# Kernel tuning notes

Hardware: AMD Instinct MI355X
Metric: run time of the kernel (lower is better)

## Reference

```python
import jax, jax.numpy as jnp
import numpy as np

B, L, D = 256, 256, 128          # batch, max_len, embedding_dim
H = W = 16                       # H=int(sqrt(L)), W=L//H
N, CBD = 128, 1024               # embedding_num, code_book_dim = N*8 = D*8
BETA = 0.25
BN_EPS = 1e-3                    # tf.layers.batch_normalization default


def _conv(x, w, b):
    return jax.lax.conv_general_dilated(x, w, (1, 1), 'VALID',
        dimension_numbers=('NHWC', 'HWIO', 'NHWC')) + b


def _convT(x, w, b):
    return jax.lax.conv_transpose(x, w, (1, 1), 'VALID',
        dimension_numbers=('NHWC', 'HWIO', 'NHWC')) + b


def _bn(x, g, b):
    # inference-mode BN with moving_mean=0, moving_var=1 (tf.layers default training=False)
    return g * (x * (1.0 / np.sqrt(1.0 + BN_EPS))) + b


def setup_inputs() -> dict:
    key = jax.random.key(0)
    ks = jax.random.split(key, 24)
    rn = lambda k, s, sc=0.05: (jax.random.normal(k, s, dtype=jnp.float32) * sc)
    inp = {
        'x': jax.random.normal(ks[0], (B, L, D), dtype=jnp.float32),
        'mask': jnp.ones((B, L), dtype=jnp.float32),
        'code_book': jax.random.normal(ks[1], (N, CBD), dtype=jnp.float32),
        # encoder: conv2d k=2 valid, channels D -> 2D -> 4D -> 8D
        'ew1': rn(ks[2], (2, 2, D, 2 * D)), 'eb1': jnp.zeros((2 * D,), jnp.float32),
        'eg1': jnp.ones((2 * D,), jnp.float32), 'ebt1': jnp.zeros((2 * D,), jnp.float32),
        'ew2': rn(ks[3], (2, 2, 2 * D, 4 * D)), 'eb2': jnp.zeros((4 * D,), jnp.float32),
        'eg2': jnp.ones((4 * D,), jnp.float32), 'ebt2': jnp.zeros((4 * D,), jnp.float32),
        'ew3': rn(ks[4], (2, 2, 4 * D, 8 * D)), 'eb3': jnp.zeros((8 * D,), jnp.float32),
        # decoder: conv2d_transpose k=2 valid, channels 8D -> 4D -> 2D -> D
        'dw1': rn(ks[5], (2, 2, 8 * D, 4 * D)), 'db1': jnp.zeros((4 * D,), jnp.float32),
        'dg1': jnp.ones((4 * D,), jnp.float32), 'dbt1': jnp.zeros((4 * D,), jnp.float32),
        'dw2': rn(ks[6], (2, 2, 4 * D, 2 * D)), 'db2': jnp.zeros((2 * D,), jnp.float32),
        'dg2': jnp.ones((2 * D,), jnp.float32), 'dbt2': jnp.zeros((2 * D,), jnp.float32),
        'dw3': rn(ks[7], (2, 2, 2 * D, D)), 'db3': jnp.zeros((D,), jnp.float32),
    }
    return inp


def reference(x, mask, code_book,
              ew1, eb1, eg1, ebt1, ew2, eb2, eg2, ebt2, ew3, eb3,
              dw1, db1, dg1, dbt1, dw2, db2, dg2, dbt2, dw3, db3):
    # ---- encoder (conv branch) ----
    xi = x.reshape(-1, H, W, D)                                   # [B,16,16,D]
    h = jax.nn.relu(_bn(_conv(xi, ew1, eb1), eg1, ebt1))          # [B,15,15,2D]
    h = jax.nn.relu(_bn(_conv(h, ew2, eb2), eg2, ebt2))           # [B,14,14,4D]
    x_encode = _conv(h, ew3, eb3)                                 # [B,13,13,8D]

    # ---- VQ codebook lookup (get_quantized) ----
    flat = x_encode.reshape(-1, CBD)                              # [B*169, CBD]
    dist = (jnp.sum(flat ** 2, axis=1, keepdims=True)
            + jnp.sum(code_book ** 2, axis=1)
            - 2.0 * flat @ code_book.T)                           # [B*169, N]
    idx = jnp.argmin(dist, axis=1)
    quantized = code_book[idx].reshape(x_encode.shape)            # gather == one_hot @ code_book

    # ---- straight-through + decoder ----
    ste = x_encode + jax.lax.stop_gradient(quantized - x_encode)
    h = jax.nn.relu(_bn(_convT(ste, dw1, db1), dg1, dbt1))        # [B,14,14,4D]
    h = jax.nn.relu(_bn(_convT(h, dw2, db2), dg2, dbt2))          # [B,15,15,2D]
    vq = _convT(h, dw3, db3)                                      # [B,16,16,D]
    vq_x = vq.reshape(-1, L, D)

    vq_mean = jnp.sum(vq_x, axis=1) / jnp.sum(mask, axis=-1, keepdims=True)

    recon = jnp.mean((x - vq_x) ** 2)
    vq_l = jnp.mean((quantized - jax.lax.stop_gradient(x_encode)) ** 2)
    commit = jnp.mean((x_encode - jax.lax.stop_gradient(quantized)) ** 2)
    vqvae_loss = recon + vq_l + BETA * commit
    return (vq_mean, vq_x, x_encode, quantized, vqvae_loss)
```

## Files before the change

### kernel.cpp

```cpp
#include <hip/hip_runtime.h>
#include <math.h>

typedef float f4 __attribute__((ext_vector_type(4)));
typedef short s8 __attribute__((ext_vector_type(8)));

#define WS_FLOATS 66000000L
__device__ float g_fallback[WS_FLOATS];

__device__ __forceinline__ f4 ldg4(const float* p) { return *(const f4*)p; }

__device__ __forceinline__ unsigned short bfr(float x) {
    unsigned int u = __float_as_uint(x);
    u += 0x7fffu + ((u >> 16) & 1u);
    return (unsigned short)(u >> 16);
}
__device__ __forceinline__ float bff(unsigned short h) {
    return __uint_as_float(((unsigned int)h) << 16);
}
__device__ __forceinline__ s8 z8() { s8 z = {0,0,0,0,0,0,0,0}; return z; }

__device__ __forceinline__ void split8(const f4& x0, const f4& x1, s8& hi, s8& lo) {
#pragma unroll
    for (int e = 0; e < 4; ++e) {
        unsigned short h0 = bfr(x0[e]);
        hi[e] = (short)h0; lo[e] = (short)bfr(x0[e] - bff(h0));
        unsigned short h1 = bfr(x1[e]);
        hi[e + 4] = (short)h1; lo[e + 4] = (short)bfr(x1[e] - bff(h1));
    }
}

__global__ __launch_bounds__(512, 2)
void e2_gemm(const short* __restrict__ aHi, const short* __restrict__ aLo,
             const short* __restrict__ wHi, const short* __restrict__ wLo,
             const float* __restrict__ bias, const float* __restrict__ gamma,
             const float* __restrict__ beta,
             short* __restrict__ oHi, short* __restrict__ oLo, float bns)
{
    extern __shared__ short smem[];
    const int tid = threadIdx.x;
    const int w = tid >> 6, l = tid & 63;
    const int fr = l & 15, fq = l >> 4;
    const int wm = (w >> 2) * 128;
    const int wn = (w & 3) * 32;

    int m0, n0;
    {
        const int nwg = gridDim.x;
        const int bid = blockIdx.x;
        const int q = nwg >> 3, r = nwg & 7;
        const int xcd = bid & 7, c = bid >> 3;
        const int wg = (xcd < r ? xcd * (q + 1) : r * (q + 1) + (xcd - r) * q) + c;
        m0 = (wg >> 2) * 256;
        n0 = (wg & 3) * 128;
    }

    int aBase[2], aSwz[2], aDst[2];
#pragma unroll
    for (int i = 0; i < 2; ++i) {
        int p = tid + 512 * i;
        int row = p >> 2, ch = p & 3;
        int m = m0 + row;
        int b = m / 196; int rem = m - b * 196;
        int oi = rem / 14, oj = rem - oi * 14;
        aBase[i] = ((b * 15 + oi) * 15 + oj) * 256;
        aSwz[i] = (ch ^ (row & 3)) << 3;
        aDst[i] = row * 32 + ch * 8;
    }
    const int bRow = tid >> 2, bch = tid & 3;
    const int bSrcO = (n0 + bRow) * 1024 + ((bch ^ (bRow & 3)) << 3);
    const int bDst = bRow * 32 + bch * 8;

    auto stage = [&](int sel, int kc) {
        const int t = kc >> 8;
        const int toff = ((t >> 1) * 15 + (t & 1)) * 256 + (kc & 255);
#pragma unroll
        for (int i = 0; i < 2; ++i) {
            __builtin_amdgcn_global_load_lds(
                (const __attribute__((address_space(1))) void*)(aHi + aBase[i] + toff + aSwz[i]),
                (__attribute__((address_space(3))) void*)(smem + sel * 8192 + aDst[i]), 16, 0, 0);
            __builtin_amdgcn_global_load_lds(
                (const __attribute__((address_space(1))) void*)(aLo + aBase[i] + toff + aSwz[i]),
                (__attribute__((address_space(3))) void*)(smem + 16384 + sel * 8192 + aDst[i]), 16, 0, 0);
        }
        __builtin_amdgcn_global_load_lds(
            (const __attribute__((address_space(1))) void*)(wHi + bSrcO + kc),
            (__attribute__((address_space(3))) void*)(smem + 32768 + sel * 4096 + bDst), 16, 0, 0);
        __builtin_amdgcn_global_load_lds(
            (const __attribute__((address_space(1))) void*)(wLo + bSrcO + kc),
            (__attribute__((address_space(3))) void*)(smem + 40960 + sel * 4096 + bDst), 16, 0, 0);
    };

    f4 acc[8][2];
#pragma unroll
    for (int a = 0; a < 8; ++a)
#pragma unroll
        for (int b = 0; b < 2; ++b) acc[a][b] = (f4){0.f, 0.f, 0.f, 0.f};

    stage(0, 0);
    stage(1, 32);

    for (int t = 0; t < 32; ++t) {
        const int sel = t & 1;
        if (t < 31) asm volatile("s_waitcnt vmcnt(6)" ::: "memory");
        else        asm volatile("s_waitcnt vmcnt(0)" ::: "memory");
        __builtin_amdgcn_s_barrier();
        __builtin_amdgcn_sched_barrier(0);

        const short* Ah = smem + sel * 8192;
        const short* Al = smem + 16384 + sel * 8192;
        const short* Bh = smem + 32768 + sel * 4096;
        const short* Bl = smem + 40960 + sel * 4096;

        s8 afh[8], afl[8], bfh[2], bfl[2];
#pragma unroll
        for (int mf = 0; mf < 8; ++mf) {
            int ar = wm + mf * 16 + fr;
            int ao = ar * 32 + ((fq ^ (ar & 3)) << 3);
            afh[mf] = *(const s8*)&Ah[ao];
            afl[mf] = *(const s8*)&Al[ao];
        }
#pragma unroll
        for (int nf = 0; nf < 2; ++nf) {
            int br = wn + nf * 16 + fr;
            int bo = br * 32 + ((fq ^ (br & 3)) << 3);
            bfh[nf] = *(const s8*)&Bh[bo];
            bfl[nf] = *(const s8*)&Bl[bo];
        }
        asm volatile("s_waitcnt lgkmcnt(0)" ::: "memory");
        __builtin_amdgcn_sched_barrier(0);
        __builtin_amdgcn_s_barrier();
        __builtin_amdgcn_sched_barrier(0);
        if (t + 2 < 32) stage(sel, (t + 2) * 32);

        __builtin_amdgcn_s_setprio(1);
#pragma unroll
        for (int mf = 0; mf < 8; ++mf)
#pragma unroll
            for (int nf = 0; nf < 2; ++nf) {
                acc[mf][nf] = __builtin_amdgcn_mfma_f32_16x16x32_bf16(
                    afh[mf], bfh[nf], acc[mf][nf], 0, 0, 0);
                acc[mf][nf] = __builtin_amdgcn_mfma_f32_16x16x32_bf16(
                    afh[mf], bfl[nf], acc[mf][nf], 0, 0, 0);
                acc[mf][nf] = __builtin_amdgcn_mfma_f32_16x16x32_bf16(
                    afl[mf], bfh[nf], acc[mf][nf], 0, 0, 0);
            }
        __builtin_amdgcn_s_setprio(0);
    }

    float bi2[2], ga[2], be[2];
#pragma unroll
    for (int nf = 0; nf < 2; ++nf) {
        int col = n0 + wn + nf * 16 + fr;
        bi2[nf] = bias[col]; ga[nf] = gamma[col]; be[nf] = beta[col];
    }
#pragma unroll
    for (int mf = 0; mf < 8; ++mf)
#pragma unroll
        for (int j = 0; j < 4; ++j) {
            long gm = m0 + wm + mf * 16 + fq * 4 + j;
#pragma unroll
            for (int nf = 0; nf < 2; ++nf) {
                float v = ga[nf] * ((acc[mf][nf][j] + bi2[nf]) * bns) + be[nf];
                v = fmaxf(v, 0.f);
                long o = gm * 512 + n0 + wn + nf * 16 + fr;
                unsigned short h = bfr(v);
                oHi[o] = (short)h;
                oLo[o] = (short)bfr(v - bff(h));
            }
        }
}

template<int EPI>
__global__ __launch_bounds__(512, 2)
void gemm256(const short* __restrict__ aSrc, const short* __restrict__ wHi,
             const float* __restrict__ bias, const float* __restrict__ gamma,
             const float* __restrict__ beta, void* __restrict__ oHi,
             double* __restrict__ sacc, const short* __restrict__ zsrc,
             int IH, int IW, int OHOW, int OW, int N, int K, int off,
             int ntShift, float bns)
{
    extern __shared__ short smem[];

    const int tid = threadIdx.x;
    const int w = tid >> 6;
    const int l = tid & 63;
    const int lr = l >> 3;
    const int lc = l & 7;
    const int fr = l & 15, fq = l >> 4;
    const int wm = (w >> 2) * 128;
    const int wn = (w & 3) * 64;

    int m0, n0;
    {
        const int nwg = gridDim.x;
        const int bid = blockIdx.x;
        const int q = nwg >> 3, r = nwg & 7;
        const int xcd = bid & 7, c = bid >> 3;
        const int wg = (xcd < r ? xcd * (q + 1) : r * (q + 1) + (xcd - r) * q) + c;
        const int NTm1 = (1 << ntShift) - 1;
        m0 = (wg >> ntShift) * 256;
        n0 = (wg & NTm1) * 256;
    }

    int bOff[4], oiA[4], ojA[4], bRowB[4];
#pragma unroll
    for (int i = 0; i < 4; ++i) {
        int row = (w << 5) + (i << 3) + lr;
        int m = m0 + row;
        int b = m / OHOW; int rem = m - b * OHOW;
        oiA[i] = rem / OW; ojA[i] = rem - oiA[i] * OW;
        bOff[i] = b * IH * IW;
        bRowB[i] = (n0 + row) * K;
    }
    const int swz = (lc ^ lr) << 3;

    auto stage = [&](int sel, int kc) {
        short* Ab = smem + sel * 16384;
        short* Bb = smem + 32768 + sel * 16384;
        const int t = kc >> 9;
        const int ci = (kc & 511) + swz;
        const int di = (t >> 1) + off, dj = (t & 1) + off;
#pragma unroll
        for (int i = 0; i < 4; ++i) {
            int ii = oiA[i] + di, jj = ojA[i] + dj;
            bool v = (ii >= 0) && (ii < IH) && (jj >= 0) && (jj < IW);
            const short* sA = v ? aSrc + (long)(bOff[i] + ii * IW + jj) * 512 + ci
                                : zsrc + (l << 3);
            __builtin_amdgcn_global_load_lds(
                (const __attribute__((address_space(1))) void*)sA,
                (__attribute__((address_space(3))) void*)(Ab + (((w << 5) + (i << 3)) * 64)),
                16, 0, 0);
            const short* sB = wHi + bRowB[i] + kc + swz;
            __builtin_amdgcn_global_load_lds(
                (const __attribute__((address_space(1))) void*)sB,
                (__attribute__((address_space(3))) void*)(Bb + (((w << 5) + (i << 3)) * 64)),
                16, 0, 0);
        }
    };

    f4 acc[8][4];
#pragma unroll
    for (int a = 0; a < 8; ++a)
#pragma unroll
        for (int b = 0; b < 4; ++b) acc[a][b] = (f4){0.f, 0.f, 0.f, 0.f};

    const int NT = K >> 6;
    stage(0, 0);
    stage(1, 64);

    for (int t = 0; t < NT; ++t) {
        const int sel = t & 1;
        const short* Ab = smem + sel * 16384;
        const short* Bb = smem + 32768 + sel * 16384;

        if (t < NT - 1) asm volatile("s_waitcnt vmcnt(8)" ::: "memory");
        else            asm volatile("s_waitcnt vmcnt(0)" ::: "memory");
        __builtin_amdgcn_s_barrier();
        __builtin_amdgcn_sched_barrier(0);

        s8 af[8], bf[4];
#pragma unroll
        for (int mf = 0; mf < 8; ++mf) {
            int row = wm + mf * 16 + fr;
            int c = fq ^ (row & 7);
            af[mf] = *(const s8*)&Ab[row * 64 + (c << 3)];
        }
#pragma unroll
        for (int nf = 0; nf < 4; ++nf) {
            int row = wn + nf * 16 + fr;
            int c = fq ^ (row & 7);
            bf[nf] = *(const s8*)&Bb[row * 64 + (c << 3)];
        }
        asm volatile("s_waitcnt lgkmcnt(0)" ::: "memory");
        __builtin_amdgcn_sched_barrier(0);
        __builtin_amdgcn_s_setprio(1);
#pragma unroll
        for (int mf = 0; mf < 8; ++mf)
#pragma unroll
            for (int nf = 0; nf < 4; ++nf)
                acc[mf][nf] = __builtin_amdgcn_mfma_f32_16x16x32_bf16(
                    af[mf], bf[nf], acc[mf][nf], 0, 0, 0);
        __builtin_amdgcn_s_setprio(0);

#pragma unroll
        for (int mf = 0; mf < 8; ++mf) {
            int row = wm + mf * 16 + fr;
            int c = (4 + fq) ^ (row & 7);
            af[mf] = *(const s8*)&Ab[row * 64 + (c << 3)];
        }
#pragma unroll
        for (int nf = 0; nf < 4; ++nf) {
            int row = wn + nf * 16 + fr;
            int c = (4 + fq) ^ (row & 7);
            bf[nf] = *(const s8*)&Bb[row * 64 + (c << 3)];
        }
        asm volatile("s_waitcnt lgkmcnt(0)" ::: "memory");
        __builtin_amdgcn_sched_barrier(0);
        __builtin_amdgcn_s_barrier();
        __builtin_amdgcn_sched_barrier(0);
        if (t + 2 < NT) stage(sel, (t + 2) << 6);

        __builtin_amdgcn_s_setprio(1);
#pragma unroll
        for (int mf = 0; mf < 8; ++mf)
#pragma unroll
            for (int nf = 0; nf < 4; ++nf)
                acc[mf][nf] = __builtin_amdgcn_mfma_f32_16x16x32_bf16(
                    af[mf], bf[nf], acc[mf][nf], 0, 0, 0);
        __builtin_amdgcn_s_setprio(0);
    }

    if (EPI == 3) {
        float bi[4];
#pragma unroll
        for (int nf = 0; nf < 4; ++nf) bi[nf] = bias[n0 + wn + nf * 16 + fr];
        double tsum = 0.0;
#pragma unroll
        for (int mf = 0; mf < 8; ++mf)
#pragma unroll
            for (int j = 0; j < 4; ++j) {
                long gm = m0 + wm + mf * 16 + fq * 4 + j;
                float* orow = (float*)oHi + gm * (long)N + n0;
#pragma unroll
                for (int nf = 0; nf < 4; ++nf) {
                    float v = acc[mf][nf][j] + bi[nf];
                    orow[wn + nf * 16 + fr] = v;
                    tsum += (double)v * v;
                }
            }
        __syncthreads();
        double* rd = (double*)smem;
        rd[tid] = tsum; __syncthreads();
        for (int h = 256; h; h >>= 1) {
            if (tid < h) rd[tid] += rd[tid + h];
            __syncthreads();
        }
        if (tid == 0) atomicAdd(sacc, rd[0]);
    } else {
        float bi[4], ga[4], be[4];
#pragma unroll
        for (int nf = 0; nf < 4; ++nf) {
            int col = n0 + wn + nf * 16 + fr;
            bi[nf] = bias[col]; ga[nf] = gamma[col]; be[nf] = beta[col];
        }
#pragma unroll
        for (int mf = 0; mf < 8; ++mf)
#pragma unroll
            for (int j = 0; j < 4; ++j) {
                long gm = m0 + wm + mf * 16 + fq * 4 + j;
                short* orow = (short*)oHi + gm * (long)N + n0;
#pragma unroll
                for (int nf = 0; nf < 4; ++nf) {
                    float v = ga[nf] * ((acc[mf][nf][j] + bi[nf]) * bns) + be[nf];
                    orow[wn + nf * 16 + fr] = (short)bfr(fmaxf(v, 0.f));
                }
            }
    }
}

template<int SPLIT, int ASRC, int EPI, int OUTF>
__global__ __launch_bounds__(256, 2)
void mfma_conv(const void* __restrict__ aHi, const void* __restrict__ aLo,
               const short* __restrict__ wHi, const short* __restrict__ wLo,
               const float* __restrict__ bias, const float* __restrict__ gamma,
               const float* __restrict__ beta,
               void* __restrict__ oHi, void* __restrict__ oLo,
               int* __restrict__ idxo,
               const float* __restrict__ xref, float* __restrict__ colsum,
               double* __restrict__ sacc,
               int IH, int IW, int Cin, int cinShift, int OHOW, int OW,
               int N, int K, int off, int ntShift, float bns)
{
    constexpr int PL = 128 * 64;
    constexpr int NPL = (SPLIT == 1) ? 3 : 4;
    __shared__ short smem[NPL * PL];
    short* Ah = smem;
    short* Al  = smem + PL;
    short* BhS = smem + 2 * PL;
    short* BlS = smem + 3 * PL;

    const int tid = threadIdx.x;
    const int lane = tid & 63, wid = tid >> 6;
    const int fr = lane & 15, fq = lane >> 4;
    const int wm = (wid >> 1) * 64, wn = (wid & 1) * 64;

    int m0, n0;
    {
        const int nwg = gridDim.x;
        const int bid = blockIdx.x;
        const int q = nwg >> 3, r = nwg & 7;
        const int xcd = bid & 7, c = bid >> 3;
        const int wg = (xcd < r ? xcd * (q + 1) : r * (q + 1) + (xcd - r) * q) + c;
        const int NTm1 = (1 << ntShift) - 1;
        m0 = (wg >> ntShift) * 128;
        n0 = (wg & NTm1) * 128;
    }

    const int sr = tid >> 1;
    const int skh = (tid & 1) << 5;

    long tapOff[4]; bool tv[4];
    {
        int m = m0 + sr;
        int b = m / OHOW; int rem = m - b * OHOW;
        int oi = rem / OW; int oj = rem - oi * OW;
#pragma unroll
        for (int t = 0; t < 4; ++t) {
            int ii = oi + (t >> 1) + off, jj = oj + (t & 1) + off;
            bool v = (ii >= 0) && (ii < IH) && (jj >= 0) && (jj < IW);
            tv[t] = v;
            tapOff[t] = ((long)b * IH + (v ? ii : 0)) * IW + (v ? jj : 0);
        }
    }

    f4 acc[4][4];
#pragma unroll
    for (int a = 0; a < 4; ++a)
#pragma unroll
        for (int b = 0; b < 4; ++b) acc[a][b] = (f4){0.f, 0.f, 0.f, 0.f};

    const short* wHrow = wHi + (long)(n0 + sr) * K;
    const short* wLrow = (SPLIT == 2) ? (wLo + (long)(n0 + sr) * K) : nullptr;

    const int swzW = (sr & 7) << 3;
    const int sbase = sr * 64;

    s8 rah[4], ral[4], rbh[4], rbl[4];
    f4 rax0[4], rax1[4];

    auto LOADREGS = [&](int kc) {
        const int kk = kc + skh;
        const int t = kk >> cinShift;
        const int ci = kk & (Cin - 1);
        const bool v = tv[t];
        if (ASRC == 0) {
            const float* p = (const float*)aHi + tapOff[t] * Cin + ci;
#pragma unroll
            for (int q = 0; q < 4; ++q) {
                rax0[q] = v ? ldg4(p + 8 * q) : (f4){0.f,0.f,0.f,0.f};
                rax1[q] = v ? ldg4(p + 8 * q + 4) : (f4){0.f,0.f,0.f,0.f};
            }
        } else if (ASRC == 1) {
            const short* ph = (const short*)aHi + tapOff[t] * Cin + ci;
            const short* pl = (const short*)aLo + tapOff[t] * Cin + ci;
#pragma unroll
            for (int q = 0; q < 4; ++q) {
                rah[q] = v ? *(const s8*)(ph + 8 * q) : z8();
                ral[q] = v ? *(const s8*)(pl + 8 * q) : z8();
            }
        } else {
            const short* ph = (const short*)aHi + tapOff[t] * Cin + ci;
#pragma unroll
            for (int q = 0; q < 4; ++q) rah[q] = v ? *(const s8*)(ph + 8 * q) : z8();
        }
        if (SPLIT == 2) {
#pragma unroll
            for (int q = 0; q < 4; ++q) {
                rbh[q] = *(const s8*)(wHrow + kc + skh + 8 * q);
                rbl[q] = *(const s8*)(wLrow + kc + skh + 8 * q);
            }
        }
    };

    auto STORE = [&]() {
        if (ASRC == 0) {
#pragma unroll
            for (int q = 0; q < 4; ++q) split8(rax0[q], rax1[q], rah[q], ral[q]);
        }
#pragma unroll
        for (int q = 0; q < 4; ++q) {
            int kx = (skh + 8 * q) ^ swzW;
            *(s8*)&Ah[sbase + kx] = rah[q];
            if (SPLIT == 2) {
                *(s8*)&Al[sbase + kx]  = ral[q];
                *(s8*)&BhS[sbase + kx] = rbh[q];
                *(s8*)&BlS[sbase + kx] = rbl[q];
            }
        }
    };

    auto stageB = [&](int bsel, int kc2) {
        short* bb = smem + (1 + bsel) * PL;
        const int rr0 = wid << 5;
#pragma unroll
        for (int i = 0; i < 4; ++i) {
            const int r = rr0 + 8 * i + (lane >> 3);
            const int c = lane & 7;
            const short* src = wHi + (long)(n0 + r) * K + kc2 + 8 * (c ^ (r & 7));
            __builtin_amdgcn_global_load_lds(
                (const __attribute__((address_space(1))) void*)src,
                (__attribute__((address_space(3))) void*)(bb + (rr0 + 8 * i) * 64),
                16, 0, 0);
        }
    };

    int bcur = 0;
    LOADREGS(0);
    if (SPLIT == 1) stageB(0, 0);

    for (int kc = 0; kc < K; kc += 64) {
        if (SPLIT == 1) {
            asm volatile("s_waitcnt lgkmcnt(0)" ::: "memory");
            __builtin_amdgcn_s_barrier();
            STORE();
            if (kc + 64 < K) {
                stageB(bcur ^ 1, kc + 64);
                asm volatile("s_waitcnt vmcnt(4)" ::: "memory");
            } else {
                asm volatile("s_waitcnt vmcnt(0)" ::: "memory");
            }
            __builtin_amdgcn_sched_barrier(0);
            asm volatile("s_waitcnt lgkmcnt(0)" ::: "memory");
            __builtin_amdgcn_s_barrier();
        } else {
            __syncthreads();
            STORE();
            __syncthreads();
        }
        if (kc + 64 < K) LOADREGS(kc + 64);

        const short* Bc = (SPLIT == 1) ? (smem + (1 + bcur) * PL) : BhS;

        __builtin_amdgcn_s_setprio(1);
#pragma unroll
        for (int ks = 0; ks < 2; ++ks) {
            const int colk = ks * 32 + fq * 8;
            s8 afh[4], afl[4], bfh[4], bfl[4];
#pragma unroll
            for (int mf = 0; mf < 4; ++mf) {
                int ar = wm + mf * 16 + fr;
                int ai = ar * 64 + (colk ^ ((ar & 7) << 3));
                afh[mf] = *(const s8*)&Ah[ai];
                if (SPLIT == 2) afl[mf] = *(const s8*)&Al[ai];
            }
#pragma unroll
            for (int nf = 0; nf < 4; ++nf) {
                int br = wn + nf * 16 + fr;
                int bi2 = br * 64 + (colk ^ ((br & 7) << 3));
                bfh[nf] = *(const s8*)&Bc[bi2];
                if (SPLIT == 2) bfl[nf] = *(const s8*)&BlS[bi2];
            }
#pragma unroll
            for (int mf = 0; mf < 4; ++mf)
#pragma unroll
                for (int nf = 0; nf < 4; ++nf) {
                    acc[mf][nf] = __builtin_amdgcn_mfma_f32_16x16x32_bf16(
                        afh[mf], bfh[nf], acc[mf][nf], 0, 0, 0);
                    if (SPLIT == 2) {
                        acc[mf][nf] = __builtin_amdgcn_mfma_f32_16x16x32_bf16(
                            afh[mf], bfl[nf], acc[mf][nf], 0, 0, 0);
                        acc[mf][nf] = __builtin_amdgcn_mfma_f32_16x16x32_bf16(
                            afl[mf], bfh[nf], acc[mf][nf], 0, 0, 0);
                    }
                }
        }
        __builtin_amdgcn_s_setprio(0);
        bcur ^= 1;
    }

    if (EPI == 2) {
        __syncthreads();
        float* pbv = (float*)smem;
        int*   piv = (int*)((float*)smem + 256);
        float cnv[4];
#pragma unroll
        for (int nf = 0; nf < 4; ++nf) cnv[nf] = bias[n0 + wn + nf * 16 + fr];
#pragma unroll
        for (int mf = 0; mf < 4; ++mf)
#pragma unroll
            for (int j = 0; j < 4; ++j) {
                float best = 3.4e38f; int bi = 0;
#pragma unroll
                for (int nf = 0; nf < 4; ++nf) {
                    float d = cnv[nf] - 2.0f * acc[mf][nf][j];
                    int col = wn + nf * 16 + fr;
                    if (d < best) { best = d; bi = col; }
                }
#pragma unroll
                for (int sh = 1; sh <= 8; sh <<= 1) {
                    float ov = __shfl_xor(best, sh, 64);
                    int ob = __shfl_xor(bi, sh, 64);
                    if (ov < best || (ov == best && ob < bi)) { best = ov; bi = ob; }
                }
                if (fr == 0) {
                    int r = wm + mf * 16 + fq * 4 + j;
                    pbv[(wid & 1) * 128 + r] = best;
                    piv[(wid & 1) * 128 + r] = bi;
                }
            }
        __syncthreads();
        double win = 0.0;
        if (tid < 128) {
            float b0 = pbv[tid], b1 = pbv[128 + tid];
            int i0 = piv[tid], i1 = piv[128 + tid];
            idxo[m0 + tid] = (b1 < b0) ? i1 : i0;
            win = (double)((b1 < b0) ? b1 : b0);
        }
        __syncthreads();
        double* rd = (double*)smem;
        rd[tid] = win; __syncthreads();
        for (int h = 128; h; h >>= 1) {
            if (tid < h) rd[tid] += rd[tid + h];
            __syncthreads();
        }
        if (tid == 0) atomicAdd(sacc, rd[0]);
        return;
    }

    float bi[4], ga[4], be[4];
#pragma unroll
    for (int nf = 0; nf < 4; ++nf) {
        int col = n0 + wn + nf * 16 + fr;
        bi[nf] = bias[col];
        if (EPI == 1) { ga[nf] = gamma[col]; be[nf] = beta[col]; }
    }
    double tsum = 0.0;
    float csum[4] = {0.f, 0.f, 0.f, 0.f};
#pragma unroll
    for (int mf = 0; mf < 4; ++mf)
#pragma unroll
        for (int j = 0; j < 4; ++j) {
            long gm = m0 + wm + mf * 16 + fq * 4 + j;
#pragma unroll
            for (int nf = 0; nf < 4; ++nf) {
                int col = n0 + wn + nf * 16 + fr;
                float vv = acc[mf][nf][j] + bi[nf];
                if (EPI == 1) {
                    vv = ga[nf] * (vv * bns) + be[nf];
                    vv = fmaxf(vv, 0.f);
                }
                long o = gm * (long)N + col;
                if (OUTF == 0) {
                    ((float*)oHi)[o] = vv;
                } else if (OUTF == 2) {
                    ((short*)oHi)[o] = (short)bfr(vv);
                } else {
                    unsigned short h = bfr(vv);
                    ((short*)oHi)[o] = (short)h;
                    ((short*)oLo)[o] = (short)bfr(vv - bff(h));
                }
                if (EPI == 3) tsum += (double)vv * vv;
                if (EPI == 4) {
                    float d = vv - xref[o];
                    tsum += (double)d * d;
                    csum[nf] += vv;
                }
            }
        }
    if (EPI == 4) {
        int bb128 = (m0 >> 8) * 128;
#pragma unroll
        for (int nf = 0; nf < 4; ++nf)
            atomicAdd(&colsum[bb128 + n0 + wn + nf * 16 + fr], csum[nf]);
    }
    if (EPI == 3 || EPI == 4) {
        __syncthreads();
        double* rd = (double*)smem;
        rd[tid] = tsum; __syncthreads();
        for (int h = 128; h; h >>= 1) {
            if (tid < h) rd[tid] += rd[tid + h];
            __syncthreads();
        }
        if (tid == 0) atomicAdd(sacc, rd[0]);
    }
}

__global__ void prep_all(const float* __restrict__ ew1, const float* __restrict__ ew2,
                         const float* __restrict__ ew3, const float* __restrict__ dw1,
                         const float* __restrict__ dw2, const float* __restrict__ dw3,
                         const float* __restrict__ cb,
                         short* __restrict__ ewt1h, short* __restrict__ ewt1l,
                         short* __restrict__ ewt2h, short* __restrict__ ewt2l,
                         short* __restrict__ ewt3h,
                         short* __restrict__ dwt1Th, short* __restrict__ dwt1Tl,
                         short* __restrict__ dwt2h, short* __restrict__ dwt3h,
                         short* __restrict__ cbh, short* __restrict__ cbl,
                         float* __restrict__ zbuf)
{
    int b = blockIdx.x;
    int t = threadIdx.x;
    if (b < 512) {
        int i = b * 256 + t; int n = i >> 9, k = i & 511;
        float x = ew1[(long)k * 256 + n]; unsigned short h = bfr(x);
        ewt1h[i] = (short)h; ewt1l[i] = (short)bfr(x - bff(h));
    } else if (b < 2560) {
        int i = (b - 512) * 256 + t; int n = i >> 10, k = i & 1023;
        float x = ew2[(long)k * 512 + n]; unsigned short h = bfr(x);
        ewt2h[i] = (short)h; ewt2l[i] = (short)bfr(x - bff(h));
    } else if (b < 10752) {
        int i = (b - 2560) * 256 + t; int n = i >> 11, k = i & 2047;
        ewt3h[i] = (short)bfr(ew3[(long)k * 1024 + n]);
    } else if (b < 18944) {
        int i = (b - 10752) * 256 + t; int Np = i >> 10, co = i & 1023;
        int tt = Np >> 9, nn = Np & 511;
        float x = dw1[((long)(tt * 1024 + co)) * 512 + nn]; unsigned short h = bfr(x);
        dwt1Th[i] = (short)h; dwt1Tl[i] = (short)bfr(x - bff(h));
    } else if (b < 20992) {
        int i = (b - 18944) * 256 + t; int n = i >> 11, k = i & 2047;
        dwt2h[i] = (short)bfr(dw2[(long)k * 256 + n]);
    } else if (b < 21504) {
        int i = (b - 20992) * 256 + t; int n = i >> 10, k = i & 1023;
        dwt3h[i] = (short)bfr(dw3[(long)k * 128 + n]);
    } else if (b < 22016) {
        int i = (b - 21504) * 256 + t;
        float x = cb[i]; unsigned short h = bfr(x);
        cbh[i] = (short)h; cbl[i] = (short)bfr(x - bff(h));
    } else {
        int i = (b - 22016) * 256 + t; if (i < 2048) zbuf[i] = 0.f;
    }
}

__global__ void wsplitT(const float* __restrict__ p1, short* __restrict__ hi,
                        short* __restrict__ lo)
{
    int i = blockIdx.x * 256 + threadIdx.x;
    if (i >= 262144) return;
    int n = i >> 11, k = i & 2047;
    float x = p1[(long)k * 128 + n];
    unsigned short h = bfr(x);
    hi[i] = (short)h;
    lo[i] = (short)bfr(x - bff(h));
}

__global__ void code_bias(const float* __restrict__ cb, const float* __restrict__ eb3,
                          float* __restrict__ bias2)
{
    int c = blockIdx.x * 4 + (threadIdx.x >> 6);
    int lane = threadIdx.x & 63;
    if (c >= 128) return;
    const f4* p = (const f4*)(cb + (long)c * 1024);
    const f4* e = (const f4*)eb3;
    float s2 = 0.f, su = 0.f;
#pragma unroll
    for (int q = 0; q < 4; ++q) {
        f4 v = p[q * 64 + lane];
        f4 w = e[q * 64 + lane];
        s2 += (v[0]*v[0] + v[1]*v[1]) + (v[2]*v[2] + v[3]*v[3]);
        su += (v[0]*w[0] + v[1]*w[1]) + (v[2]*w[2] + v[3]*w[3]);
    }
#pragma unroll
    for (int sh = 32; sh; sh >>= 1) {
        s2 += __shfl_xor(s2, sh, 64);
        su += __shfl_xor(su, sh, 64);
    }
    if (lane == 0) bias2[c] = s2 - 2.f * su;
}

__global__ __launch_bounds__(256)
void d1_gather(const float* __restrict__ CD, const int* __restrict__ idx,
               const float* __restrict__ db1, const float* __restrict__ dg1,
               const float* __restrict__ dbt1, short* __restrict__ out, float bns)
{
    int m = blockIdx.x * 4 + (threadIdx.x >> 6);
    int lane = threadIdx.x & 63;
    if (m >= 50176) return;
    int b = m / 196, rem = m - b * 196;
    int oi = rem / 14, oj = rem - oi * 14;
    float2 acc[4];
#pragma unroll
    for (int q = 0; q < 4; ++q) acc[q] = make_float2(0.f, 0.f);
#pragma unroll
    for (int t = 0; t < 4; ++t) {
        int ii = oi - 1 + (t >> 1), jj = oj - 1 + (t & 1);
        if (ii >= 0 && ii < 13 && jj >= 0 && jj < 13) {
            int c = idx[(b * 13 + ii) * 13 + jj];
            const float2* p = (const float2*)(CD + ((long)c * 2048 + t * 512));
#pragma unroll
            for (int q = 0; q < 4; ++q) {
                float2 v = p[lane + 64 * q];
                acc[q].x += v.x; acc[q].y += v.y;
            }
        }
    }
#pragma unroll
    for (int q = 0; q < 4; ++q) {
        int n = 2 * (lane + 64 * q);
        float v0 = fmaxf(dg1[n]     * ((acc[q].x + db1[n])     * bns) + dbt1[n],     0.f);
        float v1 = fmaxf(dg1[n + 1] * ((acc[q].y + db1[n + 1]) * bns) + dbt1[n + 1], 0.f);
        short2 s2v;
        s2v.x = (short)bfr(v0); s2v.y = (short)bfr(v1);
        ((short2*)out)[(long)m * 256 + lane + 64 * q] = s2v;
    }
}

__global__ void gather_rows(const float* __restrict__ cb, const int* __restrict__ idx,
                            float* __restrict__ q)
{
    int m = blockIdx.x;
    int c = idx[m];
    const f4* src = (const f4*)(cb + (long)c * 1024);
    f4* dst = (f4*)(q + (long)m * 1024);
    dst[threadIdx.x] = src[threadIdx.x];
}

__global__ void finalize2(const double* __restrict__ s, float* __restrict__ loss)
{
    if (threadIdx.x == 0)
        loss[0] = (float)(s[0] / 8388608.0 + 1.25 * ((s[1] + s[2]) / 44302336.0));
}

__global__ void vq_mean_fin(const float* __restrict__ colsum,
                            const float* __restrict__ mask, float* __restrict__ o)
{
    __shared__ float red[128];
    int b = blockIdx.x;
    int d = threadIdx.x;
    red[d] = mask[b * 256 + d] + mask[b * 256 + 128 + d];
    __syncthreads();
    for (int h = 64; h; h >>= 1) { if (d < h) red[d] += red[d + h]; __syncthreads(); }
    o[b * 128 + d] = colsum[b * 128 + d] / red[0];
}

extern "C" void kernel_launch(void* const* d_in, const int* in_sizes, int n_in,
                              void* d_out, int out_size, void* d_ws, size_t ws_size,
                              hipStream_t stream)
{
    const float* x    = (const float*)d_in[0];
    const float* mask = (const float*)d_in[1];
    const float* cb   = (const float*)d_in[2];
    const float* ew1 = (const float*)d_in[3];
    const float* eb1 = (const float*)d_in[4];
    const float* eg1 = (const float*)d_in[5];
    const float* ebt1= (const float*)d_in[6];
    const float* ew2 = (const float*)d_in[7];
    const float* eb2 = (const float*)d_in[8];
    const float* eg2 = (const float*)d_in[9];
    const float* ebt2= (const float*)d_in[10];
    const float* ew3 = (const float*)d_in[11];
    const float* eb3 = (const float*)d_in[12];
    const float* dw1 = (const float*)d_in[13];
    const float* db1 = (const float*)d_in[14];
    const float* dg1 = (const float*)d_in[15];
    const float* dbt1= (const float*)d_in[16];
    const float* dw2 = (const float*)d_in[17];
    const float* db2 = (const float*)d_in[18];
    const float* dg2 = (const float*)d_in[19];
    const float* dbt2= (const float*)d_in[20];
    const float* dw3 = (const float*)d_in[21];
    const float* db3 = (const float*)d_in[22];

    float* out = (float*)d_out;
    float* o_vqmean = out;
    float* o_vqx    = out + 32768;
    float* o_xe     = out + 8421376;
    float* o_q      = out + 52723712;
    float* o_loss   = out + 97026048;

    float* base;
    if (ws_size >= (size_t)WS_FLOATS * 4) {
        base = (float*)d_ws;
    } else {
        void* p = nullptr;
        hipGetSymbolAddress(&p, HIP_SYMBOL(g_fallback));
        base = (float*)p;
    }

    float* cur = base;
    short* h1h = (short*)cur; cur += 7372800;
    short* h1l = (short*)cur; cur += 7372800;
    short* h2h = (short*)cur; cur += 12845056;
    short* h2l = (short*)cur; cur += 12845056;
    short* d1o = (short*)cur; cur += 12845056;
    short* d2o = (short*)cur; cur += 7372800;
    short* ewt1h = (short*)cur; cur += 65536;
    short* ewt1l = (short*)cur; cur += 65536;
    short* ewt2h = (short*)cur; cur += 262144;
    short* ewt2l = (short*)cur; cur += 262144;
    short* ewt3h = (short*)cur; cur += 1048576;
    short* dwt1Th = (short*)cur; cur += 1048576;
    short* dwt1Tl = (short*)cur; cur += 1048576;
    short* dwt2h = (short*)cur; cur += 262144;
    short* dwt3h = (short*)cur; cur += 65536;
    short* cbh   = (short*)cur; cur += 65536;
    short* cbl   = (short*)cur; cur += 65536;
    float* P1raw = cur; cur += 262144;
    short* wvh   = (short*)cur; cur += 131072;
    short* wvl   = (short*)cur; cur += 131072;
    float* CDt   = cur; cur += 262144;
    float* bias2 = cur; cur += 128;
    float* zbuf  = cur; cur += 2048;
    int* idxb = (int*)cur; cur += 43264;
    float* colsum = cur; cur += 32768;
    double* sdbl = (double*)cur; cur += 16;

    const float bns = (float)(1.0 / sqrt(1.0 + 1e-3));

    hipFuncSetAttribute(reinterpret_cast<const void*>(&gemm256<3>),
                        hipFuncAttributeMaxDynamicSharedMemorySize, 131072);
    hipFuncSetAttribute(reinterpret_cast<const void*>(&gemm256<1>),
                        hipFuncAttributeMaxDynamicSharedMemorySize, 131072);
    hipFuncSetAttribute(reinterpret_cast<const void*>(&e2_gemm),
                        hipFuncAttributeMaxDynamicSharedMemorySize, 98304);

    hipMemsetAsync(colsum, 0, 32768 * sizeof(float), stream);
    hipMemsetAsync(sdbl, 0, 3 * sizeof(double), stream);
    prep_all<<<22024, 256, 0, stream>>>(ew1, ew2, ew3, dw1, dw2, dw3, cb,
        ewt1h, ewt1l, ewt2h, ewt2l, ewt3h, dwt1Th, dwt1Tl, dwt2h, dwt3h,
        cbh, cbl, zbuf);
    code_bias<<<32, 256, 0, stream>>>(cb, eb3, bias2);

    mfma_conv<2, 0, 0, 0><<<16, 256, 0, stream>>>(
        ew3, nullptr, cbh, cbl, zbuf, nullptr, nullptr, P1raw, nullptr, nullptr,
        nullptr, nullptr, nullptr,
        2, 2050, 1024, 10, 2048, 2048, 128, 1024, 0, 0, bns);
    wsplitT<<<1024, 256, 0, stream>>>(P1raw, wvh, wvl);
    mfma_conv<2, 0, 0, 0><<<16, 256, 0, stream>>>(
        cb, nullptr, dwt1Th, dwt1Tl, zbuf, nullptr, nullptr, CDt, nullptr, nullptr,
        nullptr, nullptr, nullptr,
        2, 130, 1024, 10, 128, 128, 2048, 1024, 0, 4, bns);

    mfma_conv<2, 0, 1, 1><<<900, 256, 0, stream>>>(
        x, nullptr, ewt1h, ewt1l, eb1, eg1, ebt1, h1h, h1l, nullptr,
        nullptr, nullptr, nullptr,
        16, 16, 128, 7, 225, 15, 256, 512, 0, 1, bns);
    e2_gemm<<<784, 512, 98304, stream>>>(
        h1h, h1l, ewt2h, ewt2l, eb2, eg2, ebt2, h2h, h2l, bns);
    gemm256<3><<<676, 512, 131072, stream>>>(
        h2h, ewt3h, eb3, nullptr, nullptr, o_xe, sdbl + 1, (const short*)zbuf,
        14, 14, 169, 13, 1024, 2048, 0, 2, bns);

    mfma_conv<2, 1, 2, 0><<<338, 256, 0, stream>>>(
        h2h, h2l, wvh, wvl, bias2, nullptr, nullptr, nullptr, nullptr, idxb,
        nullptr, nullptr, sdbl + 2,
        14, 14, 512, 9, 169, 13, 128, 2048, 0, 0, bns);
    gather_rows<<<43264, 256, 0, stream>>>(cb, idxb, o_q);

    d1_gather<<<12544, 256, 0, stream>>>(CDt, idxb, db1, dg1, dbt1, d1o, bns);
    gemm256<1><<<225, 512, 131072, stream>>>(
        d1o, dwt2h, db2, dg2, dbt2, d2o, nullptr, (const short*)zbuf,
        14, 14, 225, 15, 256, 2048, -1, 0, bns);
    mfma_conv<1, 2, 4, 0><<<512, 256, 0, stream>>>(
        d2o, nullptr, dwt3h, nullptr, db3, nullptr, nullptr, o_vqx, nullptr, nullptr,
        x, colsum, sdbl + 0,
        15, 15, 256, 8, 256, 16, 128, 1024, -1, 0, bns);

    vq_mean_fin<<<256, 128, 0, stream>>>(colsum, mask, o_vqmean);
    finalize2<<<1, 64, 0, stream>>>(sdbl, o_loss);
}
```

Baseline: 939.4 us.

## Rebalance e2_gemm warp tiling to 64x64 and interleave hi/lo planes in LDS

After: 909.9 us. -3.1%, faster.

```diff
diff --git a/kernel.cpp b/kernel.cpp
--- a/kernel.cpp
+++ b/kernel.cpp
@@ -40,8 +40,8 @@
     const int tid = threadIdx.x;
     const int w = tid >> 6, l = tid & 63;
     const int fr = l & 15, fq = l >> 4;
-    const int wm = (w >> 2) * 128;
-    const int wn = (w & 3) * 32;
+    const int wm = (w >> 1) * 64;
+    const int wn = (w & 1) * 64;
 
     int m0, n0;
     {
@@ -54,47 +54,52 @@
         n0 = (wg & 3) * 128;
     }
 
-    int aBase[2], aSwz[2], aDst[2];
-#pragma unroll
-    for (int i = 0; i < 2; ++i) {
-        int p = tid + 512 * i;
-        int row = p >> 2, ch = p & 3;
+    const int lrow8 = l >> 3;
+    const int u = (l & 7) ^ lrow8;
+    const short* aPlane = (u & 4) ? aLo : aHi;
+    const short* wPlane = (u & 4) ? wLo : wHi;
+    const int srcC = (u & 3) << 3;
+
+    int aBase[4];
+#pragma unroll
+    for (int i = 0; i < 4; ++i) {
+        int row = w * 32 + i * 8 + lrow8;
         int m = m0 + row;
         int b = m / 196; int rem = m - b * 196;
         int oi = rem / 14, oj = rem - oi * 14;
-        aBase[i] = ((b * 15 + oi) * 15 + oj) * 256;
-        aSwz[i] = (ch ^ (row & 3)) << 3;
-        aDst[i] = row * 32 + ch * 8;
-    }
-    const int bRow = tid >> 2, bch = tid & 3;
-    const int bSrcO = (n0 + bRow) * 1024 + ((bch ^ (bRow & 3)) << 3);
-    const int bDst = bRow * 32 + bch * 8;
+        aBase[i] = ((b * 15 + oi) * 15 + oj) * 256 + srcC;
+    }
+    int bBase[2];
+#pragma unroll
+    for (int j = 0; j < 2; ++j) {
+        int r2 = w * 16 + j * 8 + lrow8;
+        bBase[j] = (n0 + r2) * 1024 + srcC;
+    }
 
     auto stage = [&](int sel, int kc) {
         const int t = kc >> 8;
         const int toff = ((t >> 1) * 15 + (t & 1)) * 256 + (kc & 255);
-#pragma unroll
-        for (int i = 0; i < 2; ++i) {
+        short* Ab = smem + sel * 16384;
+        short* Bb = smem + 32768 + sel * 8192;
+#pragma unroll
+        for (int i = 0; i < 4; ++i)
             __builtin_amdgcn_global_load_lds(
-                (const __attribute__((address_space(1))) void*)(aHi + aBase[i] + toff + aSwz[i]),
-                (__attribute__((address_space(3))) void*)(smem + sel * 8192 + aDst[i]), 16, 0, 0);
+                (const __attribute__((address_space(1))) void*)(aPlane + aBase[i] + toff),
+                (__attribute__((address_space(3))) void*)(Ab + (w * 32 + i * 8) * 64),
+                16, 0, 0);
+#pragma unroll
+        for (int j = 0; j < 2; ++j)
             __builtin_amdgcn_global_load_lds(
-                (const __attribute__((address_space(1))) void*)(aLo + aBase[i] + toff + aSwz[i]),
-                (__attribute__((address_space(3))) void*)(smem + 16384 + sel * 8192 + aDst[i]), 16, 0, 0);
-        }
-        __builtin_amdgcn_global_load_lds(
-            (const __attribute__((address_space(1))) void*)(wHi + bSrcO + kc),
-            (__attribute__((address_space(3))) void*)(smem + 32768 + sel * 4096 + bDst), 16, 0, 0);
-        __builtin_amdgcn_global_load_lds(
-            (const __attribute__((address_space(1))) void*)(wLo + bSrcO + kc),
-            (__attribute__((address_space(3))) void*)(smem + 40960 + sel * 4096 + bDst), 16, 0, 0);
+                (const __attribute__((address_space(1))) void*)(wPlane + bBase[j] + kc),
+                (__attribute__((address_space(3))) void*)(Bb + (w * 16 + j * 8) * 64),
+                16, 0, 0);
     };
 
-    f4 acc[8][2];
-#pragma unroll
-    for (int a = 0; a < 8; ++a)
-#pragma unroll
-        for (int b = 0; b < 2; ++b) acc[a][b] = (f4){0.f, 0.f, 0.f, 0.f};
+    f4 acc[4][4];
+#pragma unroll
+    for (int a = 0; a < 4; ++a)
+#pragma unroll
+        for (int b = 0; b < 4; ++b) acc[a][b] = (f4){0.f, 0.f, 0.f, 0.f};
 
     stage(0, 0);
     stage(1, 32);
@@ -106,25 +111,23 @@
         __builtin_amdgcn_s_barrier();
         __builtin_amdgcn_sched_barrier(0);
 
-        const short* Ah = smem + sel * 8192;
-        const short* Al = smem + 16384 + sel * 8192;
-        const short* Bh = smem + 32768 + sel * 4096;
-        const short* Bl = smem + 40960 + sel * 4096;
-
-        s8 afh[8], afl[8], bfh[2], bfl[2];
-#pragma unroll
-        for (int mf = 0; mf < 8; ++mf) {
+        const short* Ab = smem + sel * 16384;
+        const short* Bb = smem + 32768 + sel * 8192;
+
+        s8 afh[4], afl[4], bfh[4], bfl[4];
+#pragma unroll
+        for (int mf = 0; mf < 4; ++mf) {
             int ar = wm + mf * 16 + fr;
-            int ao = ar * 32 + ((fq ^ (ar & 3)) << 3);
-            afh[mf] = *(const s8*)&Ah[ao];
-            afl[mf] = *(const s8*)&Al[ao];
-        }
-#pragma unroll
-        for (int nf = 0; nf < 2; ++nf) {
+            int sw = ar & 7;
+            afh[mf] = *(const s8*)&Ab[ar * 64 + ((fq ^ sw) << 3)];
+            afl[mf] = *(const s8*)&Ab[ar * 64 + (((4 + fq) ^ sw) << 3)];
+        }
+#pragma unroll
+        for (int nf = 0; nf < 4; ++nf) {
             int br = wn + nf * 16 + fr;
-            int bo = br * 32 + ((fq ^ (br & 3)) << 3);
-            bfh[nf] = *(const s8*)&Bh[bo];
-            bfl[nf] = *(const s8*)&Bl[bo];
+            int sw = br & 7;
+            bfh[nf] = *(const s8*)&Bb[br * 64 + ((fq ^ sw) << 3)];
+            bfl[nf] = *(const s8*)&Bb[br * 64 + (((4 + fq) ^ sw) << 3)];
         }
         asm volatile("s_waitcnt lgkmcnt(0)" ::: "memory");
         __builtin_amdgcn_sched_barrier(0);
@@ -134,9 +137,9 @@
 
         __builtin_amdgcn_s_setprio(1);
 #pragma unroll
-        for (int mf = 0; mf < 8; ++mf)
-#pragma unroll
-            for (int nf = 0; nf < 2; ++nf) {
+        for (int mf = 0; mf < 4; ++mf)
+#pragma unroll
+            for (int nf = 0; nf < 4; ++nf) {
                 acc[mf][nf] = __builtin_amdgcn_mfma_f32_16x16x32_bf16(
                     afh[mf], bfh[nf], acc[mf][nf], 0, 0, 0);
                 acc[mf][nf] = __builtin_amdgcn_mfma_f32_16x16x32_bf16(
@@ -147,19 +150,19 @@
         __builtin_amdgcn_s_setprio(0);
     }
 
-    float bi2[2], ga[2], be[2];
-#pragma unroll
-    for (int nf = 0; nf < 2; ++nf) {
+    float bi2[4], ga[4], be[4];
+#pragma unroll
+    for (int nf = 0; nf < 4; ++nf) {
         int col = n0 + wn + nf * 16 + fr;
         bi2[nf] = bias[col]; ga[nf] = gamma[col]; be[nf] = beta[col];
     }
 #pragma unroll
-    for (int mf = 0; mf < 8; ++mf)
+    for (int mf = 0; mf < 4; ++mf)
 #pragma unroll
         for (int j = 0; j < 4; ++j) {
             long gm = m0 + wm + mf * 16 + fq * 4 + j;
 #pragma unroll
-            for (int nf = 0; nf < 2; ++nf) {
+            for (int nf = 0; nf < 4; ++nf) {
                 float v = ga[nf] * ((acc[mf][nf][j] + bi2[nf]) * bns) + be[nf];
                 v = fmaxf(v, 0.f);
                 long o = gm * 512 + n0 + wn + nf * 16 + fr;
```
